# Optimization experiments

Measured on AMD Instinct MI355X. Metric: run time of the kernel, lower is better.

The kernel has to match this reference:

```python
import jax, jax.numpy as jnp
import numpy as np
from jax import lax

WS = 11          # window_size
SIGMA = 1.5
CH = 3
PAD = WS // 2


def _depthwise_conv(x, w, groups):
    # x: [B, C, H, W], w: [C_out, C_in/groups, kh, kw]
    return lax.conv_general_dilated(
        x, w, window_strides=(1, 1), padding=[(PAD, PAD), (PAD, PAD)],
        feature_group_count=groups,
        dimension_numbers=("NCHW", "OIHW", "NCHW"))


def _make_window():
    xs = jnp.arange(WS, dtype=jnp.float32) - (WS // 2)
    g = jnp.exp(-(xs ** 2) / (2.0 * SIGMA ** 2))
    g = g / g.sum()
    w2d = jnp.outer(g, g)                       # [WS, WS]
    return jnp.broadcast_to(w2d, (CH, 1, WS, WS))  # depthwise kernel


def setup_inputs() -> dict:
    key = jax.random.key(0)
    k1, k2, k3 = jax.random.split(key, 3)
    B, H, W = 16, 512, 512
    img1 = jax.random.uniform(k1, (B, CH, H, W), dtype=jnp.float32)
    img2 = jax.random.uniform(k2, (B, CH, H, W), dtype=jnp.float32)
    match = jax.random.uniform(k3, (B, 1, H, W), dtype=jnp.float32)
    return {"img1": img1, "img2": img2, "match": match}


def reference(img1, img2, match):
    window = _make_window()
    box = jnp.ones((1, 1, WS, WS), dtype=jnp.float32) / (WS * WS)

    # mask from match map: box-filter then threshold
    m = _depthwise_conv(match, box, 1) + 1e-07
    mask = (m > 0.5).astype(jnp.float32) + 1e-07   # [B,1,H,W]

    mu1 = _depthwise_conv(img1, window, CH)
    mu2 = _depthwise_conv(img2, window, CH)
    mu1_sq = mu1 * mu1
    mu2_sq = mu2 * mu2
    mu1_mu2 = mu1 * mu2
    sigma1_sq = _depthwise_conv(img1 * img1, window, CH) - mu1_sq
    sigma2_sq = _depthwise_conv(img2 * img2, window, CH) - mu2_sq
    sigma12 = _depthwise_conv(img1 * img2, window, CH) - mu1_mu2

    C1 = 0.01 ** 2
    C2 = 0.03 ** 2
    ssim_map = ((2 * mu1_mu2 + C1) * (2 * sigma12 + C2)) / (
        (mu1_sq + mu2_sq + C1) * (sigma1_sq + sigma2_sq + C2))

    # mask [B,1,H,W] broadcasts over the 3 channels of ssim_map
    return jnp.sum((1.0 - ssim_map) * mask) / jnp.sum(mask) / 3.0
```

## Files before the change

### kernel.cpp

```cpp
#include <hip/hip_runtime.h>


#define BATCH 16
#define CHANS 3
#define IMH 512
#define IMW 512
#define STRIPW 64
#define STRIPH 64
#define RINGR 18
#define LDSW 84
#define SUP 8
#define NSUP (STRIPH / SUP)
#define NQ 20

#define MTW 64
#define MTH 64
#define MRAWH 74

__device__ __forceinline__ float4 ld4s(const float* p) { return *(const float4*)p; }
__device__ __forceinline__ void st4s(float* p, float4 v) { *(float4*)p = v; }
__device__ __forceinline__ void fma4(float4& a, float w, float4 x) {
    a.x = fmaf(w, x.x, a.x); a.y = fmaf(w, x.y, a.y);
    a.z = fmaf(w, x.z, a.z); a.w = fmaf(w, x.w, a.w);
}
__device__ __forceinline__ void fma4m(float4& a, float w, float4 x, float4 y) {
    a.x = fmaf(w, x.x * y.x, a.x); a.y = fmaf(w, x.y * y.y, a.y);
    a.z = fmaf(w, x.z * y.z, a.z); a.w = fmaf(w, x.w * y.w, a.w);
}
__device__ __forceinline__ void add4(float4& a, float4 x) {
    a.x += x.x; a.y += x.y; a.z += x.z; a.w += x.w;
}

__device__ __forceinline__ void convg4s(const float* __restrict__ row, int cb,
                                        const float* __restrict__ g, float out[4]) {
    out[0] = 0.0f; out[1] = 0.0f; out[2] = 0.0f; out[3] = 0.0f;
    #pragma unroll
    for (int i = 0; i < 5; ++i) {
        float4 v = ld4s(row + cb + 4 * i);
        float vv[4] = {v.x, v.y, v.z, v.w};
        #pragma unroll
        for (int e = 0; e < 4; ++e) {
            const int m = 4 * i + e;
            #pragma unroll
            for (int j = 0; j < 4; ++j) {
                const int k = m - 3 - j;
                if (k >= 0 && k <= 10)
                    out[j] = fmaf(g[k], vv[e], out[j]);
            }
        }
    }
}

__device__ __forceinline__ void convg(const float* __restrict__ row, int cb,
                                      const float* __restrict__ g, float out[4]) {
    float w[20];
    #pragma unroll
    for (int i = 0; i < 5; ++i) {
        float4 v = ld4s(row + cb + 4 * i);
        w[4*i+0] = v.x; w[4*i+1] = v.y; w[4*i+2] = v.z; w[4*i+3] = v.w;
    }
    #pragma unroll
    for (int j = 0; j < 4; ++j) {
        float a = 0.0f;
        #pragma unroll
        for (int k = 0; k < 11; ++k) a = fmaf(g[k], w[3 + j + k], a);
        out[j] = a;
    }
}

__device__ __forceinline__ void convb(const float* __restrict__ row, int cb,
                                      float out[4]) {
    float w[20];
    #pragma unroll
    for (int i = 0; i < 5; ++i) {
        float4 v = ld4s(row + cb + 4 * i);
        w[4*i+0] = v.x; w[4*i+1] = v.y; w[4*i+2] = v.z; w[4*i+3] = v.w;
    }
    #pragma unroll
    for (int j = 0; j < 4; ++j) {
        float a = 0.0f;
        #pragma unroll
        for (int k = 0; k < 11; ++k) a += w[3 + j + k];
        out[j] = a;
    }
}

__global__ __launch_bounds__(256) void mask_pass(
    const float* __restrict__ match, unsigned char* __restrict__ maskbuf,
    double* __restrict__ acc)
{
    __shared__ __align__(16) float raw[MRAWH][LDSW];
    __shared__ __align__(16) float vs[MTH][LDSW];
    __shared__ float red[4];

    const int tid = threadIdx.x;
    const int b = blockIdx.z;
    const int x0 = blockIdx.x * MTW - 8;
    const int y0 = blockIdx.y * MTH - 5;
    const float* pm = match + (size_t)b * (IMH * IMW);

    for (int t = tid; t < MRAWH * NQ; t += 256) {
        int r = t / NQ, q = t - r * NQ;
        int gy = y0 + r;
        int gx = x0 + 4 * q;
        float4 v = make_float4(0.f, 0.f, 0.f, 0.f);
        if ((unsigned)gy < IMH) {
            if ((unsigned)gx <= (IMW - 4)) {
                v = ld4s(pm + gy * IMW + gx);
            } else {
                float tmp[4];
                #pragma unroll
                for (int e = 0; e < 4; ++e) {
                    int x = gx + e;
                    bool ok = (unsigned)x < IMW;
                    tmp[e] = ok ? pm[gy * IMW + x] : 0.0f;
                }
                v = make_float4(tmp[0], tmp[1], tmp[2], tmp[3]);
            }
        }
        st4s(&raw[r][4 * q], v);
    }
    __syncthreads();

    for (int t = tid; t < MTH * NQ; t += 256) {
        int r = t / NQ, q = t - r * NQ;
        int cq = 4 * q;
        float4 a = make_float4(0.f, 0.f, 0.f, 0.f);
        #pragma unroll
        for (int k = 0; k < 11; ++k) add4(a, ld4s(&raw[r + k][cq]));
        st4s(&vs[r][cq], a);
    }
    __syncthreads();

    float den = 0.0f;
    for (int t = tid; t < MTH * 16; t += 256) {
        int r = t >> 4, q = t & 15;
        float mb[4];
        convb(vs[r], 4 * q, mb);
        unsigned char bits[4];
        #pragma unroll
        for (int j = 0; j < 4; ++j) {
            float m = mb[j] * (1.0f / 121.0f) + 1e-7f;
            bool on = m > 0.5f;
            bits[j] = (unsigned char)on;
            den += on ? (1.0f + 1e-7f) : 1e-7f;
        }
        int gy = blockIdx.y * MTH + r;
        int gx = blockIdx.x * MTW + 4 * q;
        *(uchar4*)(maskbuf + ((size_t)b << 18) + (gy << 9) + gx) =
            make_uchar4(bits[0], bits[1], bits[2], bits[3]);
    }

    for (int off = 32; off > 0; off >>= 1) den += __shfl_down(den, off);
    if ((tid & 63) == 0) red[tid >> 6] = den;
    __syncthreads();
    if (tid == 0)
        atomicAdd(&acc[1], (double)(red[0] + red[1] + red[2] + red[3]));
}

__global__ __launch_bounds__(256, 4) void ssim_main_pm(
    const float* __restrict__ img1, const float* __restrict__ img2,
    const unsigned char* __restrict__ maskbuf,
    const float* __restrict__ gw, double* __restrict__ acc)
{
    __shared__ __align__(16) float ring1[RINGR][LDSW];
    __shared__ __align__(16) float ring2[RINGR][LDSW];
    __shared__ __align__(16) float fld[5][SUP][LDSW];
    __shared__ float redn[4];

    const int tid = threadIdx.x;
    const int bc = blockIdx.z;
    const int b = bc / CHANS;
    const int c = bc - b * CHANS;
    const int ystart = blockIdx.y * STRIPH;
    const int bxg = blockIdx.x;
    const int bx0 = bxg * STRIPW - 8;

    const float* p1 = img1 + (size_t)(b * CHANS + c) * (IMH * IMW);
    const float* p2 = img2 + (size_t)(b * CHANS + c) * (IMH * IMW);
    const unsigned char* pmk = maskbuf + ((size_t)b << 18);

    float g[11];
    #pragma unroll
    for (int i = 0; i < 11; ++i) g[i] = gw[i];

    float num = 0.0f;
    const bool colsafe = (bx0 >= 0) && (bx0 + 4 * NQ <= IMW);

    auto stage = [&](int gy0, int nrows) {
        if (tid < nrows * NQ) {
            int r = tid / NQ, q = tid - r * NQ;
            int gy = gy0 + r;
            int slot = (gy + 36) % RINGR;
            int gx = bx0 + 4 * q;
            float4 v1 = make_float4(0.f, 0.f, 0.f, 0.f), v2 = v1;
            if ((unsigned)gy < IMH) {
                if (colsafe || (unsigned)gx <= (IMW - 4)) {
                    v1 = ld4s(p1 + gy * IMW + gx);
                    v2 = ld4s(p2 + gy * IMW + gx);
                } else {
                    float t1[4], t2[4];
                    #pragma unroll
                    for (int e = 0; e < 4; ++e) {
                        int x = gx + e;
                        bool ok = (unsigned)x < IMW;
                        int off = gy * IMW + (ok ? x : 0);
                        t1[e] = ok ? p1[off] : 0.0f;
                        t2[e] = ok ? p2[off] : 0.0f;
                    }
                    v1 = make_float4(t1[0], t1[1], t1[2], t1[3]);
                    v2 = make_float4(t2[0], t2[1], t2[2], t2[3]);
                }
            }
            st4s(&ring1[slot][4 * q], v1);
            st4s(&ring2[slot][4 * q], v2);
        }
    };

    stage(ystart - 5, 10);

    for (int s = 0; s < NSUP; ++s) {
        const int ybase = ystart + s * SUP;

        stage(ybase + 5, SUP);
        __syncthreads();

        #pragma unroll
        for (int pass = 0; pass < 2; ++pass) {
            if (pass == 0 || tid < SUP * 40 - 256) {
                const int u = tid + pass * 256;
                const int r = u / 40, hq = u - r * 40;
                const int cw = 2 * hq;
                int sr = (ybase + r + 31) % RINGR;
                float2 a1 = make_float2(0.f, 0.f), a2 = a1, a3 = a1,
                       a4 = a1, a5 = a1;
                #pragma unroll
                for (int k = 0; k < 11; ++k) {
                    float2 x1 = *(const float2*)&ring1[sr][cw];
                    float2 x2 = *(const float2*)&ring2[sr][cw];
                    float w = g[k];
                    a1.x = fmaf(w, x1.x, a1.x);        a1.y = fmaf(w, x1.y, a1.y);
                    a2.x = fmaf(w, x2.x, a2.x);        a2.y = fmaf(w, x2.y, a2.y);
                    a3.x = fmaf(w, x1.x * x1.x, a3.x); a3.y = fmaf(w, x1.y * x1.y, a3.y);
                    a4.x = fmaf(w, x2.x * x2.x, a4.x); a4.y = fmaf(w, x2.y * x2.y, a4.y);
                    a5.x = fmaf(w, x1.x * x2.x, a5.x); a5.y = fmaf(w, x1.y * x2.y, a5.y);
                    sr++; if (sr >= RINGR) sr -= RINGR;
                }
                *(float2*)&fld[0][r][cw] = a1;
                *(float2*)&fld[1][r][cw] = a2;
                *(float2*)&fld[2][r][cw] = a3;
                *(float2*)&fld[3][r][cw] = a4;
                *(float2*)&fld[4][r][cw] = a5;
            }
        }
        __syncthreads();

        if (tid < SUP * 16) {
            int r = tid >> 4, q = tid & 15;
            int cb = 4 * q;
            float mu1[4], mu2[4], m11[4], m22[4], m12[4];
            convg4s(fld[0][r], cb, g, mu1);
            convg4s(fld[1][r], cb, g, mu2);
            convg4s(fld[2][r], cb, g, m11);
            convg4s(fld[3][r], cb, g, m22);
            convg4s(fld[4][r], cb, g, m12);
            int gy = ybase + r;
            int gx = bxg * STRIPW + cb;
            uchar4 mk = *(const uchar4*)(pmk + (gy << 9) + gx);
            const unsigned char mkv[4] = {mk.x, mk.y, mk.z, mk.w};
            #pragma unroll
            for (int j = 0; j < 4; ++j) {
                float mu1s = mu1[j] * mu1[j];
                float mu2s = mu2[j] * mu2[j];
                float mu12 = mu1[j] * mu2[j];
                float sg1  = m11[j] - mu1s;
                float sg2  = m22[j] - mu2s;
                float sg12 = m12[j] - mu12;
                float ssim = ((2.0f * mu12 + 1e-4f) * (2.0f * sg12 + 9e-4f)) /
                             ((mu1s + mu2s + 1e-4f) * (sg1 + sg2 + 9e-4f));
                float mask = mkv[j] ? (1.0f + 1e-7f) : 1e-7f;
                num += (1.0f - ssim) * mask;
            }
        }
    }

    for (int off = 32; off > 0; off >>= 1) num += __shfl_down(num, off);
    if ((tid & 63) == 0) redn[tid >> 6] = num;
    __syncthreads();
    if (tid == 0)
        atomicAdd(&acc[0], (double)(redn[0] + redn[1] + redn[2] + redn[3]));
    (void)c;
}

#define FBSTRIPH 256
#define FBNSUP (FBSTRIPH / SUP)
__global__ __launch_bounds__(256) void ssim_main_fb(
    const float* __restrict__ img1, const float* __restrict__ img2,
    const float* __restrict__ match, double* __restrict__ acc)
{
    __shared__ __align__(16) float ring1[RINGR][LDSW];
    __shared__ __align__(16) float ring2[RINGR][LDSW];
    __shared__ __align__(16) float ringm[RINGR][LDSW];
    __shared__ __align__(16) float fld[6][SUP][LDSW];
    __shared__ float redn[4], redd[4];

    const int tid = threadIdx.x;
    const int bc = blockIdx.z;
    const int b = bc / CHANS;
    const int c = bc - b * CHANS;
    const int ystart = blockIdx.y * FBSTRIPH;
    const int bx0 = blockIdx.x * STRIPW - 8;

    const float* p1 = img1 + (size_t)(b * CHANS + c) * (IMH * IMW);
    const float* p2 = img2 + (size_t)(b * CHANS + c) * (IMH * IMW);
    const float* pm = match + (size_t)b * (IMH * IMW);

    float g[11];
    {
        float s = 0.0f;
        #pragma unroll
        for (int i = 0; i < 11; ++i) {
            float d = (float)(i - 5);
            g[i] = expf(-(d * d) / 4.5f);
            s += g[i];
        }
        #pragma unroll
        for (int i = 0; i < 11; ++i) g[i] /= s;
    }

    float num = 0.0f, den = 0.0f;

    auto stage = [&](int gy0, int nrows) {
        for (int t = tid; t < nrows * NQ; t += 256) {
            int r = t / NQ, q = t - r * NQ;
            int gy = gy0 + r;
            int slot = (gy + 36) % RINGR;
            int gx = bx0 + 4 * q;
            float4 v1, v2, vm;
            if ((unsigned)gy < IMH && (unsigned)gx <= (IMW - 4)) {
                v1 = ld4s(p1 + gy * IMW + gx);
                v2 = ld4s(p2 + gy * IMW + gx);
                vm = ld4s(pm + gy * IMW + gx);
            } else if ((unsigned)gy < IMH) {
                float t1[4], t2[4], tm[4];
                #pragma unroll
                for (int e = 0; e < 4; ++e) {
                    int x = gx + e;
                    bool ok = (unsigned)x < IMW;
                    int off = gy * IMW + (ok ? x : 0);
                    t1[e] = ok ? p1[off] : 0.0f;
                    t2[e] = ok ? p2[off] : 0.0f;
                    tm[e] = ok ? pm[off] : 0.0f;
                }
                v1 = make_float4(t1[0], t1[1], t1[2], t1[3]);
                v2 = make_float4(t2[0], t2[1], t2[2], t2[3]);
                vm = make_float4(tm[0], tm[1], tm[2], tm[3]);
            } else {
                v1 = v2 = vm = make_float4(0.f, 0.f, 0.f, 0.f);
            }
            st4s(&ring1[slot][4 * q], v1);
            st4s(&ring2[slot][4 * q], v2);
            st4s(&ringm[slot][4 * q], vm);
        }
    };

    stage(ystart - 5, 10);

    for (int s = 0; s < FBNSUP; ++s) {
        const int ybase = ystart + s * SUP;
        stage(ybase + 5, SUP);
        __syncthreads();

        if (tid < SUP * NQ) {
            int r = tid / NQ, q = tid - r * NQ;
            int cq = 4 * q;
            int sr = (ybase + r + 31) % RINGR;
            float4 a1 = make_float4(0,0,0,0), a2 = a1, a3 = a1,
                   a4 = a1, a5 = a1, am = a1;
            #pragma unroll
            for (int k = 0; k < 11; ++k) {
                float4 x1 = ld4s(&ring1[sr][cq]);
                float4 x2 = ld4s(&ring2[sr][cq]);
                float4 xm = ld4s(&ringm[sr][cq]);
                float w = g[k];
                fma4(a1, w, x1);
                fma4(a2, w, x2);
                fma4m(a3, w, x1, x1);
                fma4m(a4, w, x2, x2);
                fma4m(a5, w, x1, x2);
                add4(am, xm);
                sr++; if (sr >= RINGR) sr -= RINGR;
            }
            st4s(&fld[0][r][cq], a1);
            st4s(&fld[1][r][cq], a2);
            st4s(&fld[2][r][cq], a3);
            st4s(&fld[3][r][cq], a4);
            st4s(&fld[4][r][cq], a5);
            st4s(&fld[5][r][cq], am);
        }
        __syncthreads();

        if (tid < SUP * 16) {
            int r = tid >> 4, q = tid & 15;
            int cb = 4 * q;
            float mu1[4], mu2[4], m11[4], m22[4], m12[4], mb[4];
            convg(fld[0][r], cb, g, mu1);
            convg(fld[1][r], cb, g, mu2);
            convg(fld[2][r], cb, g, m11);
            convg(fld[3][r], cb, g, m22);
            convg(fld[4][r], cb, g, m12);
            convb(fld[5][r], cb, mb);
            #pragma unroll
            for (int j = 0; j < 4; ++j) {
                float mu1s = mu1[j] * mu1[j];
                float mu2s = mu2[j] * mu2[j];
                float mu12 = mu1[j] * mu2[j];
                float sg1  = m11[j] - mu1s;
                float sg2  = m22[j] - mu2s;
                float sg12 = m12[j] - mu12;
                float ssim = ((2.0f * mu12 + 1e-4f) * (2.0f * sg12 + 9e-4f)) /
                             ((mu1s + mu2s + 1e-4f) * (sg1 + sg2 + 9e-4f));
                float m = mb[j] * (1.0f / 121.0f) + 1e-7f;
                float mask = (m > 0.5f) ? (1.0f + 1e-7f) : 1e-7f;
                num += (1.0f - ssim) * mask;
                den += mask;
            }
        }
    }

    for (int off = 32; off > 0; off >>= 1) {
        num += __shfl_down(num, off);
        den += __shfl_down(den, off);
    }
    int wave = tid >> 6;
    int lane = tid & 63;
    if (lane == 0) { redn[wave] = num; redd[wave] = den; }
    __syncthreads();
    if (tid == 0) {
        float n = redn[0] + redn[1] + redn[2] + redn[3];
        atomicAdd(&acc[0], (double)n);
        if (c == 0) {
            float d = redd[0] + redd[1] + redd[2] + redd[3];
            atomicAdd(&acc[1], (double)d);
        }
    }
}

__global__ void init_acc(double* acc, float* gw) {
    acc[0] = 0.0;
    acc[1] = 0.0;
    if (gw != nullptr) {
        float t[11];
        float s = 0.0f;
        for (int i = 0; i < 11; ++i) {
            float d = (float)(i - 5);
            t[i] = expf(-(d * d) / 4.5f);
            s += t[i];
        }
        for (int i = 0; i < 11; ++i) gw[i] = t[i] / s;
    }
}

__global__ void finalize(const double* __restrict__ acc, float* __restrict__ out) {
    out[0] = (float)(acc[0] / acc[1] / 3.0);
}

extern "C" void kernel_launch(void* const* d_in, const int* in_sizes, int n_in,
                              void* d_out, int out_size, void* d_ws, size_t ws_size,
                              hipStream_t stream) {
    const float* img1  = (const float*)d_in[0];
    const float* img2  = (const float*)d_in[1];
    const float* match = (const float*)d_in[2];
    float* out = (float*)d_out;
    double* acc = (double*)d_ws;

    const size_t mask_need = 128 + (size_t)BATCH * IMH * IMW;
    const bool premask = (ws_size >= mask_need);
    float* gw = premask ? (float*)((char*)d_ws + 64) : nullptr;

    init_acc<<<1, 1, 0, stream>>>(acc, gw);

    dim3 block(256, 1, 1);
    if (premask) {
        unsigned char* mbuf = (unsigned char*)d_ws + 128;
        dim3 mgrid(IMW / MTW, IMH / MTH, BATCH);
        mask_pass<<<mgrid, block, 0, stream>>>(match, mbuf, acc);
        dim3 grid(IMW / STRIPW, IMH / STRIPH, BATCH * CHANS);
        ssim_main_pm<<<grid, block, 0, stream>>>(img1, img2, mbuf, gw, acc);
    } else {
        dim3 grid(IMW / STRIPW, IMH / FBSTRIPH, BATCH * CHANS);
        ssim_main_fb<<<grid, block, 0, stream>>>(img1, img2, match, acc);
    }

    finalize<<<1, 1, 0, stream>>>(acc, out);
}
```

Baseline: 240.3 us.

## Use all threads for horizontal pass, fold weight init into mask kernel

The horizontal Gaussian pass now uses all 256 threads, each computing 2 output columns, instead of 128 threads computing 4 columns. The separate init kernel is replaced by a memset of the accumulators plus weight computation inside the mask kernel. Launch bounds on the main kernel are raised from 4 to 5 blocks per SIMD to allow higher occupancy. This removes idle threads and one kernel launch, at the cost of more redundant LDS loads per output and tighter register limits.

```diff
diff --git a/kernel.cpp b/kernel.cpp
--- a/kernel.cpp
+++ b/kernel.cpp
@@ -31,26 +31,6 @@
     a.x += x.x; a.y += x.y; a.z += x.z; a.w += x.w;
 }
 
-__device__ __forceinline__ void convg4s(const float* __restrict__ row, int cb,
-                                        const float* __restrict__ g, float out[4]) {
-    out[0] = 0.0f; out[1] = 0.0f; out[2] = 0.0f; out[3] = 0.0f;
-    #pragma unroll
-    for (int i = 0; i < 5; ++i) {
-        float4 v = ld4s(row + cb + 4 * i);
-        float vv[4] = {v.x, v.y, v.z, v.w};
-        #pragma unroll
-        for (int e = 0; e < 4; ++e) {
-            const int m = 4 * i + e;
-            #pragma unroll
-            for (int j = 0; j < 4; ++j) {
-                const int k = m - 3 - j;
-                if (k >= 0 && k <= 10)
-                    out[j] = fmaf(g[k], vv[e], out[j]);
-            }
-        }
-    }
-}
-
 __device__ __forceinline__ void convg(const float* __restrict__ row, int cb,
                                       const float* __restrict__ g, float out[4]) {
     float w[20];
@@ -87,7 +67,7 @@
 
 __global__ __launch_bounds__(256) void mask_pass(
     const float* __restrict__ match, unsigned char* __restrict__ maskbuf,
-    double* __restrict__ acc)
+    float* __restrict__ gw, double* __restrict__ acc)
 {
     __shared__ __align__(16) float raw[MRAWH][LDSW];
     __shared__ __align__(16) float vs[MTH][LDSW];
@@ -98,6 +78,17 @@
     const int x0 = blockIdx.x * MTW - 8;
     const int y0 = blockIdx.y * MTH - 5;
     const float* pm = match + (size_t)b * (IMH * IMW);
+
+    if (tid == 0 && blockIdx.x == 0 && blockIdx.y == 0 && b == 0) {
+        float t[11];
+        float s = 0.0f;
+        for (int i = 0; i < 11; ++i) {
+            float d = (float)(i - 5);
+            t[i] = expf(-(d * d) / 4.5f);
+            s += t[i];
+        }
+        for (int i = 0; i < 11; ++i) gw[i] = t[i] / s;
+    }
 
     for (int t = tid; t < MRAWH * NQ; t += 256) {
         int r = t / NQ, q = t - r * NQ;
@@ -158,7 +149,7 @@
         atomicAdd(&acc[1], (double)(red[0] + red[1] + red[2] + red[3]));
 }
 
-__global__ __launch_bounds__(256, 4) void ssim_main_pm(
+__global__ __launch_bounds__(256, 5) void ssim_main_pm(
     const float* __restrict__ img1, const float* __restrict__ img2,
     const unsigned char* __restrict__ maskbuf,
     const float* __restrict__ gw, double* __restrict__ acc)
@@ -255,21 +246,34 @@
         }
         __syncthreads();
 
-        if (tid < SUP * 16) {
-            int r = tid >> 4, q = tid & 15;
-            int cb = 4 * q;
-            float mu1[4], mu2[4], m11[4], m22[4], m12[4];
-            convg4s(fld[0][r], cb, g, mu1);
-            convg4s(fld[1][r], cb, g, mu2);
-            convg4s(fld[2][r], cb, g, m11);
-            convg4s(fld[3][r], cb, g, m22);
-            convg4s(fld[4][r], cb, g, m12);
+        {
+            int r = tid >> 5, h = tid & 31;
+            const int c0 = 2 * h + 2;
+            float mu1[2], mu2[2], m11[2], m22[2], m12[2];
+            auto convg2s = [&](const float* __restrict__ row, float out[2]) {
+                float a0 = 0.0f, a1 = 0.0f;
+                #pragma unroll
+                for (int i = 0; i < 7; ++i) {
+                    float2 v = *(const float2*)(row + c0 + 2 * i);
+                    if (i >= 1 && i <= 5) a0 = fmaf(g[2*i-1], v.x, a0);
+                    if (i <= 5)           a0 = fmaf(g[2*i],   v.y, a0);
+                    if (i >= 1)           a1 = fmaf(g[2*i-2], v.x, a1);
+                    if (i >= 1 && i <= 5) a1 = fmaf(g[2*i-1], v.y, a1);
+                }
+                out[0] = a0; out[1] = a1;
+            };
+            convg2s(fld[0][r], mu1);
+            convg2s(fld[1][r], mu2);
+            convg2s(fld[2][r], m11);
+            convg2s(fld[3][r], m22);
+            convg2s(fld[4][r], m12);
+
             int gy = ybase + r;
-            int gx = bxg * STRIPW + cb;
-            uchar4 mk = *(const uchar4*)(pmk + (gy << 9) + gx);
-            const unsigned char mkv[4] = {mk.x, mk.y, mk.z, mk.w};
+            int gx = bxg * STRIPW + 2 * h;
+            uchar2 mk = *(const uchar2*)(pmk + (gy << 9) + gx);
+            const unsigned char mkv[2] = {mk.x, mk.y};
             #pragma unroll
-            for (int j = 0; j < 4; ++j) {
+            for (int j = 0; j < 2; ++j) {
                 float mu1s = mu1[j] * mu1[j];
                 float mu2s = mu2[j] * mu2[j];
                 float mu12 = mu1[j] * mu2[j];
@@ -446,21 +450,6 @@
     }
 }
 
-__global__ void init_acc(double* acc, float* gw) {
-    acc[0] = 0.0;
-    acc[1] = 0.0;
-    if (gw != nullptr) {
-        float t[11];
-        float s = 0.0f;
-        for (int i = 0; i < 11; ++i) {
-            float d = (float)(i - 5);
-            t[i] = expf(-(d * d) / 4.5f);
-            s += t[i];
-        }
-        for (int i = 0; i < 11; ++i) gw[i] = t[i] / s;
-    }
-}
-
 __global__ void finalize(const double* __restrict__ acc, float* __restrict__ out) {
     out[0] = (float)(acc[0] / acc[1] / 3.0);
 }
@@ -476,15 +465,15 @@
 
     const size_t mask_need = 128 + (size_t)BATCH * IMH * IMW;
     const bool premask = (ws_size >= mask_need);
-    float* gw = premask ? (float*)((char*)d_ws + 64) : nullptr;
-
-    init_acc<<<1, 1, 0, stream>>>(acc, gw);
+    float* gw = (float*)((char*)d_ws + 64);
+
+    hipMemsetAsync(d_ws, 0, 16, stream);
 
     dim3 block(256, 1, 1);
     if (premask) {
         unsigned char* mbuf = (unsigned char*)d_ws + 128;
         dim3 mgrid(IMW / MTW, IMH / MTH, BATCH);
-        mask_pass<<<mgrid, block, 0, stream>>>(match, mbuf, acc);
+        mask_pass<<<mgrid, block, 0, stream>>>(match, mbuf, gw, acc);
         dim3 grid(IMW / STRIPW, IMH / STRIPH, BATCH * CHANS);
         ssim_main_pm<<<grid, block, 0, stream>>>(img1, img2, mbuf, gw, acc);
     } else {
```

After: 218.0 us. 1.1x faster.
